# Kernel optimization log

Hardware: AMD Instinct MI355X
Metric: run time of the kernel (lower is better)

The kernel has to match this reference:

```python
import jax, jax.numpy as jnp
import numpy as np

N = 8192   # nodes per graph batch
D = 128    # node_feat_dim
E = 131072 # edges per graph batch
B = 64     # graphs per batch


def _linear_init(k, fin, fout):
    s = 1.0 / np.sqrt(fin)
    kw, kb = jax.random.split(k)
    W = jax.random.uniform(kw, (fin, fout), jnp.float32, -s, s)
    b = jax.random.uniform(kb, (fout,), jnp.float32, -s, s)
    return W, b


def setup_inputs() -> dict:
    key = jax.random.key(0)
    ks = jax.random.split(key, 10)
    x1 = jax.random.normal(ks[0], (N, D), jnp.float32)
    x2 = jax.random.normal(ks[1], (N, D), jnp.float32)
    edge_index1 = jax.random.randint(ks[2], (2, E), 0, N)
    edge_index2 = jax.random.randint(ks[3], (2, E), 0, N)
    # block-contiguous graph ids; every graph id present on both sides
    batch = jnp.arange(N, dtype=jnp.int32) // (N // B)
    mW1, mb1 = _linear_init(ks[4], 2 * D, 512)
    mW2, mb2 = _linear_init(ks[5], 512, 256)  # 256 == 2*D (update_net constraint)
    uW1, ub1 = _linear_init(ks[6], 4 * D, 512)
    uW2, ub2 = _linear_init(ks[7], 512, 256)
    uW3, ub3 = _linear_init(ks[8], 256, D)
    return dict(x1=x1, edge_index1=edge_index1, batch1=batch,
                x2=x2, edge_index2=edge_index2, batch2=batch,
                mW1=mW1, mb1=mb1, mW2=mW2, mb2=mb2,
                uW1=uW1, ub1=ub1, uW2=uW2, ub2=ub2, uW3=uW3, ub3=ub3)


def _message_aggr(x, edge_index, mW1, mb1, mW2, mb2):
    tgt, src = edge_index[0], edge_index[1]
    inp = jnp.concatenate([x[src], x[tgt]], axis=-1)          # [E, 2D]
    msg = jax.nn.relu(inp @ mW1 + mb1) @ mW2 + mb2            # [E, 2D]
    return jax.ops.segment_sum(msg, tgt, num_segments=x.shape[0])


def _cross_attention(x1, batch1, x2, batch2):
    scores = x1 @ x2.T                                        # [N1, N2]
    mask = batch1[:, None] == batch2[None, :]
    scores = jnp.where(mask, scores, -jnp.inf)
    att1 = x1 - jax.nn.softmax(scores, axis=1) @ x2
    att2 = x2 - jax.nn.softmax(scores, axis=0).T @ x1
    return att1, att2


def _node_update(x, messages, attentions, uW1, ub1, uW2, ub2, uW3, ub3):
    u = jnp.concatenate([messages, attentions, x], axis=-1)   # [N, 4D]
    h = jax.nn.relu(u @ uW1 + ub1)
    h = jax.nn.relu(h @ uW2 + ub2)
    return x + h @ uW3 + ub3                                  # residual update


def reference(x1, edge_index1, batch1, x2, edge_index2, batch2,
              mW1, mb1, mW2, mb2, uW1, ub1, uW2, ub2, uW3, ub3):
    m1 = _message_aggr(x1, edge_index1, mW1, mb1, mW2, mb2)
    m2 = _message_aggr(x2, edge_index2, mW1, mb1, mW2, mb2)
    a1, a2 = _cross_attention(x1, batch1, x2, batch2)
    new_x1 = _node_update(x1, m1, a1, uW1, ub1, uW2, ub2, uW3, ub3)
    new_x2 = _node_update(x2, m2, a2, uW1, ub1, uW2, ub2, uW3, ub3)
    return new_x1, new_x2
```

## Files before the change

kernel.cpp:

```cpp
#include <hip/hip_runtime.h>
#include <stdint.h>


typedef unsigned short u16;
typedef __bf16 bf16x8 __attribute__((ext_vector_type(8)));
typedef float f32x4 __attribute__((ext_vector_type(4)));

#define NN 8192
#define DD 128
#define EE 131072
#define GS 128
#define NG 64

__device__ __forceinline__ float bf2f(u16 u){
  return __uint_as_float(((uint32_t)u) << 16);
}
__device__ __forceinline__ u16 f2bf(float f){
  uint32_t x = __float_as_uint(f);
  return (u16)((x + 0x7fffu + ((x >> 16) & 1u)) >> 16);
}
__device__ __forceinline__ void gload16(const u16* g, u16* l){
  __builtin_amdgcn_global_load_lds(
      (const __attribute__((address_space(1))) uint32_t*)(uintptr_t)g,
      (__attribute__((address_space(3))) uint32_t*)(uintptr_t)l, 16, 0, 0);
}
template<int N>
__device__ __forceinline__ void wbar(){
  if constexpr (N == 0)      asm volatile("s_waitcnt vmcnt(0)" ::: "memory");
  else if constexpr (N == 1) asm volatile("s_waitcnt vmcnt(1)" ::: "memory");
  else if constexpr (N == 2) asm volatile("s_waitcnt vmcnt(2)" ::: "memory");
  else if constexpr (N == 4) asm volatile("s_waitcnt vmcnt(4)" ::: "memory");
  __builtin_amdgcn_s_barrier();
  __builtin_amdgcn_sched_barrier(0);
}
__device__ __forceinline__ void bar(){
  __builtin_amdgcn_s_barrier();
  __builtin_amdgcn_sched_barrier(0);
}

template<bool DEGBIAS, typename OT>
__device__ __forceinline__ void gemm_body(
    const u16* __restrict__ A, int lda,
    const u16* __restrict__ Wt, const float* __restrict__ bias,
    const int* __restrict__ deg,
    OT* __restrict__ out, int ldc, int K, int bx, int by,
    u16* __restrict__ sh, int t)
{
  u16* As0 = sh;         u16* Bs0 = sh + 4096;
  u16* As1 = sh + 8192;  u16* Bs1 = sh + 12288;
  const int brow = by << 7, bcol = bx << 7;
  const int w = t >> 6, lane = t & 63;
  const int rb = (w >> 1) << 6, cb = (w & 1) << 6;
  const int lr = lane & 15, lq = lane >> 4;

  f32x4 acc[4][4];
  #pragma unroll
  for (int i = 0; i < 4; i++)
    #pragma unroll
    for (int j = 0; j < 4; j++) acc[i][j] = (f32x4){0.f, 0.f, 0.f, 0.f};

  const int s0 = t, s1 = t + 256;
  const int sw0 = (((s0 & 3) ^ ((s0 >> 2) & 3)) << 3);
  const int sw1 = (((s1 & 3) ^ ((s1 >> 2) & 3)) << 3);
  const u16* Ag0 = A  + (size_t)(brow + (s0 >> 2)) * lda + sw0;
  const u16* Ag1 = A  + (size_t)(brow + (s1 >> 2)) * lda + sw1;
  const u16* Bg0 = Wt + (size_t)(bcol + (s0 >> 2)) * K   + sw0;
  const u16* Bg1 = Wt + (size_t)(bcol + (s1 >> 2)) * K   + sw1;
  const int d0 = s0 << 3, d1 = s1 << 3;

  auto stage = [&](int kb, u16* Al, u16* Bl){
    gload16(Ag0 + kb, Al + d0);
    gload16(Ag1 + kb, Al + d1);
    gload16(Bg0 + kb, Bl + d0);
    gload16(Bg1 + kb, Bl + d1);
  };
  const int swr = ((lq ^ (lr & 3)) << 3);
  auto compute = [&](const u16* Asb, const u16* Bsb){
    bf16x8 af[4], bfr[4];
    #pragma unroll
    for (int mi = 0; mi < 4; mi++)
      af[mi] = *(const bf16x8*)&Asb[(rb + mi * 16 + lr) * 32 + swr];
    #pragma unroll
    for (int ni = 0; ni < 4; ni++)
      bfr[ni] = *(const bf16x8*)&Bsb[(cb + ni * 16 + lr) * 32 + swr];
    #pragma unroll
    for (int mi = 0; mi < 4; mi++)
      #pragma unroll
      for (int ni = 0; ni < 4; ni++)
        acc[mi][ni] = __builtin_amdgcn_mfma_f32_16x16x32_bf16(af[mi], bfr[ni], acc[mi][ni], 0, 0, 0);
  };

  stage(0, As0, Bs0);
  const int half = K >> 6;
  for (int i2 = 0; i2 < half; i2++){
    const int kb = i2 << 6;
    stage(kb + 32, As1, Bs1);
    wbar<4>();
    compute(As0, Bs0);
    bar();
    if (i2 + 1 < half){
      stage(kb + 64, As0, Bs0);
      wbar<4>();
    } else {
      wbar<0>();
    }
    compute(As1, Bs1);
    bar();
  }

  #pragma unroll
  for (int mi = 0; mi < 4; mi++)
    #pragma unroll
    for (int ni = 0; ni < 4; ni++)
      #pragma unroll
      for (int rr = 0; rr < 4; rr++){
        int grow = brow + rb + mi * 16 + lq * 4 + rr;
        int gcol = bcol + cb + ni * 16 + lr;
        float v = acc[mi][ni][rr];
        if (bias) v += DEGBIAS ? (float)deg[grow] * bias[gcol] : bias[gcol];
        out[(size_t)grow * ldc + gcol] = (OT)f2bf(v);
      }
}

__device__ __forceinline__ void pq_gemm(
    const u16* __restrict__ A, const u16* __restrict__ Wt,
    const float* __restrict__ bias, u16* __restrict__ out,
    int bx, int by, u16* __restrict__ sh, int t)
{
  u16* As = sh;
  u16* Bs = sh + 16384;
  const int brow = by << 7, bcol = bx << 7;
  const int w = t >> 6, lane = t & 63;
  const int rb = (w >> 1) << 6, cb = (w & 1) << 6;
  const int lr = lane & 15, lq = lane >> 4;

  #pragma unroll
  for (int i = 0; i < 8; i++){
    int sg = i * 256 + t;
    int r = sg >> 4, p = sg & 15;
    int l = p ^ (r & 7);
    gload16(A  + (size_t)(brow + r) * 128 + (l << 3), As + sg * 8);
    gload16(Wt + (size_t)(bcol + r) * 128 + (l << 3), Bs + sg * 8);
  }
  wbar<0>();

  f32x4 acc[4][4];
  #pragma unroll
  for (int i = 0; i < 4; i++)
    #pragma unroll
    for (int j = 0; j < 4; j++) acc[i][j] = (f32x4){0.f, 0.f, 0.f, 0.f};

  #pragma unroll
  for (int kb = 0; kb < 4; kb++){
    bf16x8 af[4], bfr[4];
    #pragma unroll
    for (int mi = 0; mi < 4; mi++){
      int row = rb + mi * 16 + lr;
      af[mi] = *(const bf16x8*)&As[(row << 7) + ((((kb << 2) | lq) ^ (row & 7)) << 3)];
    }
    #pragma unroll
    for (int ni = 0; ni < 4; ni++){
      int row = cb + ni * 16 + lr;
      bfr[ni] = *(const bf16x8*)&Bs[(row << 7) + ((((kb << 2) | lq) ^ (row & 7)) << 3)];
    }
    #pragma unroll
    for (int mi = 0; mi < 4; mi++)
      #pragma unroll
      for (int ni = 0; ni < 4; ni++)
        acc[mi][ni] = __builtin_amdgcn_mfma_f32_16x16x32_bf16(af[mi], bfr[ni], acc[mi][ni], 0, 0, 0);
  }

  #pragma unroll
  for (int mi = 0; mi < 4; mi++)
    #pragma unroll
    for (int ni = 0; ni < 4; ni++)
      #pragma unroll
      for (int rr = 0; rr < 4; rr++){
        int grow = brow + rb + mi * 16 + lq * 4 + rr;
        int gcol = bcol + cb + ni * 16 + lr;
        out[(size_t)grow * 1024 + gcol] = f2bf(acc[mi][ni][rr] + bias[gcol]);
      }
}

__global__ __launch_bounds__(256)
void pre_k(const float* __restrict__ mW1, const float* __restrict__ mb1,
           const float* __restrict__ mW2, const float* __restrict__ uW1,
           const float* __restrict__ uW2, const float* __restrict__ uW3,
           const float* __restrict__ x1, const float* __restrict__ x2,
           const int* __restrict__ ei1, const int* __restrict__ ei2,
           u16* __restrict__ WtPQ, float* __restrict__ bPQ,
           u16* __restrict__ Wtm2, u16* __restrict__ Wtu1,
           u16* __restrict__ Wtu2, u16* __restrict__ Wtu3,
           u16* __restrict__ xb, u16* __restrict__ xt,
           u16* __restrict__ U, int* __restrict__ deg)
{
  __shared__ u16 T[8704];
  int b = blockIdx.x, t = threadIdx.x;
  if (b < 168){
    const float* srcs[6] = {mW1, mW1 + 128 * 512, mW2, uW1, uW2, uW3};
    u16* dsts[6] = {WtPQ, WtPQ + 512 * 128, Wtm2, Wtu1, Wtu2, Wtu3};
    const int ldSs[6] = {512, 512, 256, 512, 256, 128};
    const int ldDs[6] = {128, 128, 512, 512, 512, 256};
    const int jb[7]   = {0, 16, 32, 64, 128, 160, 168};
    int j = 0;
    while (b >= jb[j + 1]) j++;
    const int l = b - jb[j];
    const int ldS = ldSs[j], ldD = ldDs[j];
    const int ntc = ldS >> 6;
    const int k0 = (l / ntc) << 6, c0 = (l % ntc) << 6;
    const float* S = srcs[j];
    u16* D = dsts[j];
    #pragma unroll
    for (int i = 0; i < 4; i++){
      int s = i * 256 + t;
      int r = s >> 4, c4 = (s & 15) << 2;
      float4 v = *(const float4*)&S[(size_t)(k0 + r) * ldS + c0 + c4];
      uint2 pk;
      pk.x = (uint32_t)f2bf(v.x) | ((uint32_t)f2bf(v.y) << 16);
      pk.y = (uint32_t)f2bf(v.z) | ((uint32_t)f2bf(v.w) << 16);
      *(uint2*)&T[r * 68 + c4] = pk;
    }
    __syncthreads();
    #pragma unroll
    for (int i = 0; i < 4; i++){
      int s = i * 256 + t;
      int c = s >> 4, k4 = (s & 15) << 2;
      uint32_t a0 = T[(k4 + 0) * 68 + c];
      uint32_t a1 = T[(k4 + 1) * 68 + c];
      uint32_t a2 = T[(k4 + 2) * 68 + c];
      uint32_t a3 = T[(k4 + 3) * 68 + c];
      uint2 pk; pk.x = a0 | (a1 << 16); pk.y = a2 | (a3 << 16);
      *(uint2*)&D[(size_t)(c0 + c) * ldD + k0 + k4] = pk;
    }
  } else if (b == 168){
    #pragma unroll
    for (int i = 0; i < 4; i++){
      int idx = i * 256 + t;
      bPQ[idx] = (idx < 512) ? 0.f : mb1[idx - 512];
    }
  } else if (b < 2217){
    int a = b - 169;
    int side = a >> 10, blk = a & 1023;
    const float* x = side ? x2 : x1;
    int i4 = blk * 256 + t;
    float4 v = *(const float4*)&x[(size_t)i4 * 4];
    uint2 pk;
    pk.x = (uint32_t)f2bf(v.x) | ((uint32_t)f2bf(v.y) << 16);
    pk.y = (uint32_t)f2bf(v.z) | ((uint32_t)f2bf(v.w) << 16);
    *(uint2*)&xb[(size_t)side * NN * DD + (size_t)i4 * 4] = pk;
    int n = i4 >> 5, d = (i4 << 2) & 127;
    *(uint2*)&U[((size_t)side * NN + n) * 512 + 384 + d] = pk;
  } else if (b < 2473){
    int a = b - 2217;
    int side = a >> 7, blk = a & 127;
    const float* x = side ? x2 : x1;
    u16* dst = xt + (size_t)side * DD * NN;
    const int n0 = blk * 64;
    #pragma unroll
    for (int i = 0; i < 8; i++){
      int s = i * 256 + t;
      int r = s >> 5, c4 = (s & 31) << 2;
      float4 v = *(const float4*)&x[(size_t)(n0 + r) * DD + c4];
      uint2 pk;
      pk.x = (uint32_t)f2bf(v.x) | ((uint32_t)f2bf(v.y) << 16);
      pk.y = (uint32_t)f2bf(v.z) | ((uint32_t)f2bf(v.w) << 16);
      *(uint2*)&T[r * 136 + c4] = pk;
    }
    __syncthreads();
    #pragma unroll
    for (int i = 0; i < 8; i++){
      int s = i * 256 + t;
      int d = s >> 4, n4 = (s & 15) << 2;
      uint32_t a0 = T[(n4 + 0) * 136 + d];
      uint32_t a1 = T[(n4 + 1) * 136 + d];
      uint32_t a2 = T[(n4 + 2) * 136 + d];
      uint32_t a3 = T[(n4 + 3) * 136 + d];
      uint2 pk; pk.x = a0 | (a1 << 16); pk.y = a2 | (a3 << 16);
      *(uint2*)(dst + (size_t)d * NN + n0 + n4) = pk;
    }
  } else {
    int a = b - 2473;
    int side = a >> 9, blk = a & 511;
    const int* ei = side ? ei2 : ei1;
    int e = blk * 256 + t;
    atomicAdd(&deg[side * NN + ei[e]], 1);
  }
}

__global__ __launch_bounds__(256)
void scan_k(const int* __restrict__ deg,
            int* __restrict__ offs1, int* __restrict__ cur1,
            int* __restrict__ offs2, int* __restrict__ cur2){
  const int* d = deg + blockIdx.x * NN;
  int* offs = blockIdx.x ? offs2 : offs1;
  int* cur  = blockIdx.x ? cur2  : cur1;
  __shared__ int part[256];
  const int t = threadIdx.x;
  const int base = t * 32;
  int loc[32];
  int s = 0;
  #pragma unroll
  for (int i = 0; i < 32; i++){ loc[i] = s; s += d[base + i]; }
  part[t] = s;
  __syncthreads();
  for (int off = 1; off < 256; off <<= 1){
    int v = (t >= off) ? part[t - off] : 0;
    __syncthreads();
    part[t] += v;
    __syncthreads();
  }
  int pre = (t == 0) ? 0 : part[t - 1];
  #pragma unroll
  for (int i = 0; i < 32; i++){
    int o = pre + loc[i];
    offs[base + i] = o;
    cur[base + i]  = o;
  }
  if (t == 255) offs[NN] = part[255];
}

__global__ __launch_bounds__(256)
void mid_k(const u16* __restrict__ xb, const u16* __restrict__ WtPQ,
           const float* __restrict__ bPQ, u16* __restrict__ PQ,
           const int* __restrict__ ei1, const int* __restrict__ ei2,
           int* __restrict__ cur1, int* __restrict__ cur2,
           int* __restrict__ srt1, int* __restrict__ srt2)
{
  __shared__ u16 sh[32768];
  const int b = blockIdx.x, t = threadIdx.x;
  if (b < 1024){
    pq_gemm(xb, WtPQ, bPQ, PQ, b >> 7, b & 127, sh, t);
  } else {
    int a = b - 1024;
    int side = a >> 9, blk = a & 511;
    const int* ei = side ? ei2 : ei1;
    int* cur = side ? cur2 : cur1;
    int* srt = side ? srt2 : srt1;
    int e = blk * 256 + t;
    int tgt = ei[e], src = ei[EE + e];
    int p = atomicAdd(&cur[tgt], 1);
    srt[p] = src;
  }
}

__global__ __launch_bounds__(256)
void gather_k(const int* __restrict__ offs1, const int* __restrict__ srt1,
              const int* __restrict__ offs2, const int* __restrict__ srt2,
              const u16* __restrict__ PQ, u16* __restrict__ S)
{
  const int side = blockIdx.y;
  const int* offs = side ? offs2 : offs1;
  const int* srt  = side ? srt2  : srt1;
  const u16* base = PQ + (size_t)side * NN * 1024;
  u16* Sb = S + (size_t)side * NN * 512;

  const int node = (blockIdx.x << 2) + (threadIdx.x >> 6);
  const int lane = threadIdx.x & 63;
  const int beg = offs[node], end = offs[node + 1];
  const u16* lbase = base + (lane << 3);

  uint4 qv = *(const uint4*)(base + (size_t)node * 1024 + 512 + (lane << 3));
  float q[8];
  {
    uint32_t qw[4] = {qv.x, qv.y, qv.z, qv.w};
    #pragma unroll
    for (int i = 0; i < 4; i++){
      q[i * 2]     = bf2f((u16)(qw[i] & 0xffffu));
      q[i * 2 + 1] = bf2f((u16)(qw[i] >> 16));
    }
  }
  float acc[8] = {0.f,0.f,0.f,0.f,0.f,0.f,0.f,0.f};

  int e = beg;
  for (; e + 15 < end; e += 16){
    int sx[16];
    #pragma unroll
    for (int i = 0; i < 16; i++) sx[i] = srt[e + i];
    uint4 pv[16];
    #pragma unroll
    for (int i = 0; i < 16; i++)
      pv[i] = *(const uint4*)(lbase + (size_t)sx[i] * 1024);
    #pragma unroll
    for (int i = 0; i < 16; i++){
      uint32_t w0[4] = {pv[i].x, pv[i].y, pv[i].z, pv[i].w};
      #pragma unroll
      for (int j = 0; j < 4; j++){
        acc[j*2]   += fmaxf(bf2f((u16)(w0[j] & 0xffffu)) + q[j*2],   0.f);
        acc[j*2+1] += fmaxf(bf2f((u16)(w0[j] >> 16))     + q[j*2+1], 0.f);
      }
    }
  }
  for (; e + 7 < end; e += 8){
    int sx[8];
    #pragma unroll
    for (int i = 0; i < 8; i++) sx[i] = srt[e + i];
    uint4 pv[8];
    #pragma unroll
    for (int i = 0; i < 8; i++)
      pv[i] = *(const uint4*)(lbase + (size_t)sx[i] * 1024);
    #pragma unroll
    for (int i = 0; i < 8; i++){
      uint32_t w0[4] = {pv[i].x, pv[i].y, pv[i].z, pv[i].w};
      #pragma unroll
      for (int j = 0; j < 4; j++){
        acc[j*2]   += fmaxf(bf2f((u16)(w0[j] & 0xffffu)) + q[j*2],   0.f);
        acc[j*2+1] += fmaxf(bf2f((u16)(w0[j] >> 16))     + q[j*2+1], 0.f);
      }
    }
  }
  for (; e + 3 < end; e += 4){
    int sx[4];
    #pragma unroll
    for (int i = 0; i < 4; i++) sx[i] = srt[e + i];
    uint4 pv[4];
    #pragma unroll
    for (int i = 0; i < 4; i++)
      pv[i] = *(const uint4*)(lbase + (size_t)sx[i] * 1024);
    #pragma unroll
    for (int i = 0; i < 4; i++){
      uint32_t w0[4] = {pv[i].x, pv[i].y, pv[i].z, pv[i].w};
      #pragma unroll
      for (int j = 0; j < 4; j++){
        acc[j*2]   += fmaxf(bf2f((u16)(w0[j] & 0xffffu)) + q[j*2],   0.f);
        acc[j*2+1] += fmaxf(bf2f((u16)(w0[j] >> 16))     + q[j*2+1], 0.f);
      }
    }
  }
  for (; e < end; e++){
    int sA = srt[e];
    uint4 pA = *(const uint4*)(lbase + (size_t)sA * 1024);
    uint32_t aw[4] = {pA.x, pA.y, pA.z, pA.w};
    #pragma unroll
    for (int i = 0; i < 4; i++){
      acc[i*2]   += fmaxf(bf2f((u16)(aw[i] & 0xffffu)) + q[i*2],   0.f);
      acc[i*2+1] += fmaxf(bf2f((u16)(aw[i] >> 16))     + q[i*2+1], 0.f);
    }
  }
  uint4 pk;
  pk.x = (uint32_t)f2bf(acc[0]) | ((uint32_t)f2bf(acc[1]) << 16);
  pk.y = (uint32_t)f2bf(acc[2]) | ((uint32_t)f2bf(acc[3]) << 16);
  pk.z = (uint32_t)f2bf(acc[4]) | ((uint32_t)f2bf(acc[5]) << 16);
  pk.w = (uint32_t)f2bf(acc[6]) | ((uint32_t)f2bf(acc[7]) << 16);
  *(uint4*)(Sb + (size_t)node * 512 + (lane << 3)) = pk;
}

__global__ __launch_bounds__(256)
void msgattn_k(const u16* __restrict__ S, const u16* __restrict__ Wtm2,
               const float* __restrict__ mb2, const int* __restrict__ deg,
               const u16* __restrict__ xb, const u16* __restrict__ xt,
               u16* __restrict__ U)
{
  __shared__ u16 sh[26112];
  const int b = blockIdx.x, t = threadIdx.x;
  if (b < 256){
    gemm_body<true,u16>(S, 512, Wtm2, mb2, deg,
                        U, 512, 512, b >> 7, b & 127, sh, t);
    return;
  }
  const int a = b - 256;
  const int side = a >> 7;
  const int g = a & 63, h = (a >> 6) & 1;
  const u16* Xa = xb + (size_t)side * NN * DD;
  const u16* Xb = xb + (size_t)(1 - side) * NN * DD;
  const u16* Xt = xt + (size_t)(1 - side) * DD * NN;
  u16* Uside = U + (size_t)side * NN * 512;

  u16* XaS = sh;
  u16* XbS = sh + 8704;

  const int w = t >> 6, lane = t & 63;
  const int lr = lane & 15, lq = lane >> 4;

  {
    const u16* sa = Xa + ((size_t)g * GS + h * 64) * DD;
    #pragma unroll
    for (int i = 0; i < 4; i++){
      int s = i * 256 + t; int r = s >> 4, c8 = (s & 15) << 3;
      *(uint4*)&XaS[r * 136 + c8] = *(const uint4*)(sa + (size_t)r * DD + c8);
    }
    const u16* sb = Xb + (size_t)g * GS * DD;
    #pragma unroll
    for (int i = 0; i < 8; i++){
      int s = i * 256 + t; int r = s >> 4, c8 = (s & 15) << 3;
      *(uint4*)&XbS[r * 136 + c8] = *(const uint4*)(sb + (size_t)r * DD + c8);
    }
  }
  __syncthreads();

  f32x4 sc[8];
  #pragma unroll
  for (int ct = 0; ct < 8; ct++) sc[ct] = (f32x4){0.f, 0.f, 0.f, 0.f};
  #pragma unroll
  for (int kb = 0; kb < 4; kb++){
    bf16x8 aa = *(const bf16x8*)&XaS[(w * 16 + lr) * 136 + kb * 32 + (lq << 3)];
    #pragma unroll
    for (int ct = 0; ct < 8; ct++){
      bf16x8 bb = *(const bf16x8*)&XbS[(ct * 16 + lr) * 136 + kb * 32 + (lq << 3)];
      sc[ct] = __builtin_amdgcn_mfma_f32_16x16x32_bf16(aa, bb, sc[ct], 0, 0, 0);
    }
  }
  float inv[4];
  #pragma unroll
  for (int rr = 0; rr < 4; rr++){
    float m = sc[0][rr];
    #pragma unroll
    for (int ct = 1; ct < 8; ct++) m = fmaxf(m, sc[ct][rr]);
    #pragma unroll
    for (int sh_ = 1; sh_ < 16; sh_ <<= 1) m = fmaxf(m, __shfl_xor(m, sh_, 64));
    float s = 0.f;
    #pragma unroll
    for (int ct = 0; ct < 8; ct++){
      float e = __expf(sc[ct][rr] - m);
      sc[ct][rr] = e; s += e;
    }
    #pragma unroll
    for (int sh_ = 1; sh_ < 16; sh_ <<= 1) s += __shfl_xor(s, sh_, 64);
    inv[rr] = 1.f / s;
  }
  #pragma unroll
  for (int ct = 0; ct < 8; ct++)
    #pragma unroll
    for (int rr = 0; rr < 4; rr++)
      XaS[(w * 16 + lq * 4 + rr) * 136 + ct * 16 + lr] = f2bf(sc[ct][rr] * inv[rr]);
  __syncthreads();

  f32x4 o[8];
  #pragma unroll
  for (int ct = 0; ct < 8; ct++) o[ct] = (f32x4){0.f, 0.f, 0.f, 0.f};
  #pragma unroll
  for (int kb = 0; kb < 4; kb++){
    bf16x8 aa = *(const bf16x8*)&XaS[(w * 16 + lr) * 136 + kb * 32 + (lq << 3)];
    #pragma unroll
    for (int ct = 0; ct < 8; ct++){
      bf16x8 bb = *(const bf16x8*)(Xt + (size_t)(ct * 16 + lr) * NN + g * GS + kb * 32 + (lq << 3));
      o[ct] = __builtin_amdgcn_mfma_f32_16x16x32_bf16(aa, bb, o[ct], 0, 0, 0);
    }
  }
  const u16* XaG = Xa + ((size_t)g * GS + h * 64) * DD;
  #pragma unroll
  for (int ct = 0; ct < 8; ct++)
    #pragma unroll
    for (int rr = 0; rr < 4; rr++){
      int row = w * 16 + lq * 4 + rr, col = ct * 16 + lr;
      float xa = bf2f(XaG[(size_t)row * DD + col]);
      Uside[((size_t)g * GS + h * 64 + row) * 512 + 256 + col] = f2bf(xa - o[ct][rr]);
    }
}

__global__ __launch_bounds__(512)
void upd_k(const u16* __restrict__ U,
           const u16* __restrict__ Wtu1, const float* __restrict__ ub1,
           const u16* __restrict__ Wtu2, const float* __restrict__ ub2,
           const u16* __restrict__ Wtu3, const float* __restrict__ ub3,
           const float* __restrict__ x1, const float* __restrict__ x2,
           float* __restrict__ out)
{
  __shared__ u16 sh[66560];
  u16* H1s  = sh;
  u16* H2s  = sh + 33280;
  u16* Bst0 = sh + 50176;
  u16* Bst1 = sh + 58368;

  const int t = threadIdx.x;
  const int w = t >> 6, lane = t & 63;
  const int wr = w >> 2, wc = w & 3;
  const int lr = lane & 15, lq = lane >> 4;
  const int r0 = blockIdx.x << 6;

  const int sB0 = t, sB1 = t + 512;
  const int cB0 = sB0 >> 2, cB1 = sB1 >> 2;
  const int swB0 = (((sB0 & 3) ^ (cB0 & 3)) << 3);
  const int swB1 = (((sB1 & 3) ^ (cB1 & 3)) << 3);
  const int swr = ((lq ^ (lr & 3)) << 3);

  f32x4 acc[2][4];
  auto zacc = [&](){
    #pragma unroll
    for (int i = 0; i < 2; i++)
      #pragma unroll
      for (int j = 0; j < 4; j++) acc[i][j] = (f32x4){0.f, 0.f, 0.f, 0.f};
  };

  bf16x8 afA[2], afB[2];
  auto ldA = [&](int kb, bf16x8 (&af)[2]){
    #pragma unroll
    for (int mi = 0; mi < 2; mi++)
      af[mi] = *(const bf16x8*)&U[(size_t)(r0 + wr * 32 + mi * 16 + lr) * 512 + kb + (lq << 3)];
  };
  auto compA = [&](const bf16x8 (&af)[2], const u16* Bsb){
    bf16x8 bfv[4];
    #pragma unroll
    for (int ct = 0; ct < 4; ct++)
      bfv[ct] = *(const bf16x8*)&Bsb[(wc * 64 + ct * 16 + lr) * 32 + swr];
    #pragma unroll
    for (int mi = 0; mi < 2; mi++)
      #pragma unroll
      for (int ct = 0; ct < 4; ct++)
        acc[mi][ct] = __builtin_amdgcn_mfma_f32_16x16x32_bf16(af[mi], bfv[ct], acc[mi][ct], 0, 0, 0);
  };
  for (int hN = 0; hN < 2; hN++){
    zacc();
    auto stB = [&](int kb, u16* dst){
      gload16(Wtu1 + (size_t)(hN * 256 + cB0) * 512 + kb + swB0, dst + sB0 * 8);
      gload16(Wtu1 + (size_t)(hN * 256 + cB1) * 512 + kb + swB1, dst + sB1 * 8);
    };
    stB(0, Bst0);
    ldA(0, afA);
    for (int i2 = 0; i2 < 8; i2++){
      const int kb = i2 << 6;
      stB(kb + 32, Bst1); ldA(kb + 32, afB);
      wbar<4>();
      compA(afA, Bst0);
      bar();
      if (i2 < 7){
        stB(kb + 64, Bst0); ldA(kb + 64, afA);
        wbar<4>();
      } else {
        wbar<0>();
      }
      compA(afB, Bst1);
      bar();
    }
    #pragma unroll
    for (int mi = 0; mi < 2; mi++)
      #pragma unroll
      for (int ct = 0; ct < 4; ct++)
        #pragma unroll
        for (int rr = 0; rr < 4; rr++){
          int row = wr * 32 + mi * 16 + lq * 4 + rr;
          int col = wc * 64 + ct * 16 + lr;
          float v = acc[mi][ct][rr] + ub1[hN * 256 + col];
          H1s[row * 520 + hN * 256 + col] = f2bf(fmaxf(v, 0.f));
        }
  }
  __syncthreads();

  zacc();
  {
    auto stB = [&](int kb, u16* dst){
      gload16(Wtu2 + (size_t)cB0 * 512 + kb + swB0, dst + sB0 * 8);
      gload16(Wtu2 + (size_t)cB1 * 512 + kb + swB1, dst + sB1 * 8);
    };
    auto comp = [&](int kb, const u16* Bsb){
      bf16x8 af[2], bfv[4];
      #pragma unroll
      for (int mi = 0; mi < 2; mi++)
        af[mi] = *(const bf16x8*)&H1s[(wr * 32 + mi * 16 + lr) * 520 + kb + (lq << 3)];
      #pragma unroll
      for (int ct = 0; ct < 4; ct++)
        bfv[ct] = *(const bf16x8*)&Bsb[(wc * 64 + ct * 16 + lr) * 32 + swr];
      #pragma unroll
      for (int mi = 0; mi < 2; mi++)
        #pragma unroll
        for (int ct = 0; ct < 4; ct++)
          acc[mi][ct] = __builtin_amdgcn_mfma_f32_16x16x32_bf16(af[mi], bfv[ct], acc[mi][ct], 0, 0, 0);
    };
    stB(0, Bst0);
    for (int i2 = 0; i2 < 8; i2++){
      const int kb = i2 << 6;
      stB(kb + 32, Bst1);
      wbar<2>();
      comp(kb, Bst0);
      bar();
      if (i2 < 7){
        stB(kb + 64, Bst0);
        wbar<2>();
      } else {
        wbar<0>();
      }
      comp(kb + 32, Bst1);
      bar();
    }
    #pragma unroll
    for (int mi = 0; mi < 2; mi++)
      #pragma unroll
      for (int ct = 0; ct < 4; ct++)
        #pragma unroll
        for (int rr = 0; rr < 4; rr++){
          int row = wr * 32 + mi * 16 + lq * 4 + rr;
          int col = wc * 64 + ct * 16 + lr;
          H2s[row * 264 + col] = f2bf(fmaxf(acc[mi][ct][rr] + ub2[col], 0.f));
        }
  }
  __syncthreads();

  zacc();
  {
    auto stB = [&](int kb, u16* dst){
      gload16(Wtu3 + (size_t)cB0 * 256 + kb + swB0, dst + sB0 * 8);
    };
    auto comp = [&](int kb, const u16* Bsb){
      bf16x8 af[2], bfv[2];
      #pragma unroll
      for (int mi = 0; mi < 2; mi++)
        af[mi] = *(const bf16x8*)&H2s[(wr * 32 + mi * 16 + lr) * 264 + kb + (lq << 3)];
      #pragma unroll
      for (int ct = 0; ct < 2; ct++)
        bfv[ct] = *(const bf16x8*)&Bsb[(wc * 32 + ct * 16 + lr) * 32 + swr];
      #pragma unroll
      for (int mi = 0; mi < 2; mi++)
        #pragma unroll
        for (int ct = 0; ct < 2; ct++)
          acc[mi][ct] = __builtin_amdgcn_mfma_f32_16x16x32_bf16(af[mi], bfv[ct], acc[mi][ct], 0, 0, 0);
    };
    stB(0, Bst0);
    for (int i2 = 0; i2 < 4; i2++){
      const int kb = i2 << 6;
      stB(kb + 32, Bst1);
      wbar<1>();
      comp(kb, Bst0);
      bar();
      if (i2 < 3){
        stB(kb + 64, Bst0);
        wbar<1>();
      } else {
        wbar<0>();
      }
      comp(kb + 32, Bst1);
      bar();
    }
    #pragma unroll
    for (int mi = 0; mi < 2; mi++)
      #pragma unroll
      for (int ct = 0; ct < 2; ct++)
        #pragma unroll
        for (int rr = 0; rr < 4; rr++){
          int row = wr * 32 + mi * 16 + lq * 4 + rr;
          int col = wc * 32 + ct * 16 + lr;
          int grow = r0 + row;
          const float* rp = (grow < NN) ? x1 : x2;
          float v = acc[mi][ct][rr] + ub3[col]
                  + rp[(size_t)(grow & (NN - 1)) * 128 + col];
          out[(size_t)grow * 128 + col] = v;
        }
  }
}

extern "C" void kernel_launch(void* const* d_in, const int* in_sizes, int n_in,
                              void* d_out, int out_size, void* d_ws, size_t ws_size,
                              hipStream_t stream)
{
  const float* x1  = (const float*)d_in[0];
  const int*   ei1 = (const int*)  d_in[1];
  const float* x2  = (const float*)d_in[3];
  const int*   ei2 = (const int*)  d_in[4];
  const float* mW1 = (const float*)d_in[6];
  const float* mb1 = (const float*)d_in[7];
  const float* mW2 = (const float*)d_in[8];
  const float* mb2 = (const float*)d_in[9];
  const float* uW1 = (const float*)d_in[10];
  const float* ub1 = (const float*)d_in[11];
  const float* uW2 = (const float*)d_in[12];
  const float* ub2 = (const float*)d_in[13];
  const float* uW3 = (const float*)d_in[14];
  const float* ub3 = (const float*)d_in[15];
  float* out = (float*)d_out;

  char* w = (char*)d_ws;
  auto alloc = [&](size_t b){ char* p = w; w += (b + 255) & ~(size_t)255; return p; };
  u16*  S    = (u16*)alloc((size_t)2 * NN * 512 * 2);
  u16*  PQ   = (u16*)alloc((size_t)2 * NN * 1024 * 2);
  u16*  xb   = (u16*)alloc((size_t)2 * NN * DD * 2);
  u16*  xt   = (u16*)alloc((size_t)2 * DD * NN * 2);
  u16*  U    = (u16*)alloc((size_t)2 * NN * 512 * 2);
  int*  deg  = (int*)alloc((size_t)2 * NN * 4);
  int*  offs1 = (int*)alloc((NN + 1) * 4);
  int*  offs2 = (int*)alloc((NN + 1) * 4);
  int*  cur1  = (int*)alloc(NN * 4);
  int*  cur2  = (int*)alloc(NN * 4);
  int*  srt1  = (int*)alloc((size_t)EE * 4);
  int*  srt2  = (int*)alloc((size_t)EE * 4);
  u16*  WtPQ = (u16*)alloc(1024 * 128 * 2);
  float* bPQ = (float*)alloc(1024 * 4);
  u16*  Wtm2 = (u16*)alloc(256 * 512 * 2);
  u16*  Wtu1 = (u16*)alloc(512 * 512 * 2);
  u16*  Wtu2 = (u16*)alloc(256 * 512 * 2);
  u16*  Wtu3 = (u16*)alloc(128 * 256 * 2);

  hipMemsetAsync(deg, 0, (size_t)2 * NN * 4, stream);

  pre_k<<<3497, 256, 0, stream>>>(
      mW1, mb1, mW2, uW1, uW2, uW3, x1, x2, ei1, ei2,
      WtPQ, bPQ, Wtm2, Wtu1, Wtu2, Wtu3, xb, xt, U, deg);

  scan_k<<<2, 256, 0, stream>>>(deg, offs1, cur1, offs2, cur2);

  mid_k<<<2048, 256, 0, stream>>>(xb, WtPQ, bPQ, PQ, ei1, ei2,
                                  cur1, cur2, srt1, srt2);

  gather_k<<<dim3(NN / 4, 2), 256, 0, stream>>>(offs1, srt1, offs2, srt2, PQ, S);

  msgattn_k<<<512, 256, 0, stream>>>(S, Wtm2, mb2, deg, xb, xt, U);

  upd_k<<<256, 512, 0, stream>>>(U, Wtu1, ub1, Wtu2, ub2, Wtu3, ub3,
                                 x1, x2, out);
}
```

Measured before the change: 220.2 us.

## Fuse message GEMM into update kernel and move attention into mid kernel

Removes the msgattn kernel. The cross-attention blocks are appended to the mid_k launch so they run alongside the PQ GEMM and the edge sort. The message second-layer GEMM (S x Wtm2 plus degree-scaled bias) now runs at the start of upd_k, which writes U rows and then reuses them for the update MLP. This saves a launch and lets attention overlap the gather, at the cost of more work inside upd_k. Each upd_k block writes U through global memory and then reads it back within the same block, relying on that visibility being correct.

```diff
diff --git a/kernel.cpp b/kernel.cpp
--- a/kernel.cpp
+++ b/kernel.cpp
@@ -36,90 +36,6 @@
 __device__ __forceinline__ void bar(){
   __builtin_amdgcn_s_barrier();
   __builtin_amdgcn_sched_barrier(0);
-}
-
-template<bool DEGBIAS, typename OT>
-__device__ __forceinline__ void gemm_body(
-    const u16* __restrict__ A, int lda,
-    const u16* __restrict__ Wt, const float* __restrict__ bias,
-    const int* __restrict__ deg,
-    OT* __restrict__ out, int ldc, int K, int bx, int by,
-    u16* __restrict__ sh, int t)
-{
-  u16* As0 = sh;         u16* Bs0 = sh + 4096;
-  u16* As1 = sh + 8192;  u16* Bs1 = sh + 12288;
-  const int brow = by << 7, bcol = bx << 7;
-  const int w = t >> 6, lane = t & 63;
-  const int rb = (w >> 1) << 6, cb = (w & 1) << 6;
-  const int lr = lane & 15, lq = lane >> 4;
-
-  f32x4 acc[4][4];
-  #pragma unroll
-  for (int i = 0; i < 4; i++)
-    #pragma unroll
-    for (int j = 0; j < 4; j++) acc[i][j] = (f32x4){0.f, 0.f, 0.f, 0.f};
-
-  const int s0 = t, s1 = t + 256;
-  const int sw0 = (((s0 & 3) ^ ((s0 >> 2) & 3)) << 3);
-  const int sw1 = (((s1 & 3) ^ ((s1 >> 2) & 3)) << 3);
-  const u16* Ag0 = A  + (size_t)(brow + (s0 >> 2)) * lda + sw0;
-  const u16* Ag1 = A  + (size_t)(brow + (s1 >> 2)) * lda + sw1;
-  const u16* Bg0 = Wt + (size_t)(bcol + (s0 >> 2)) * K   + sw0;
-  const u16* Bg1 = Wt + (size_t)(bcol + (s1 >> 2)) * K   + sw1;
-  const int d0 = s0 << 3, d1 = s1 << 3;
-
-  auto stage = [&](int kb, u16* Al, u16* Bl){
-    gload16(Ag0 + kb, Al + d0);
-    gload16(Ag1 + kb, Al + d1);
-    gload16(Bg0 + kb, Bl + d0);
-    gload16(Bg1 + kb, Bl + d1);
-  };
-  const int swr = ((lq ^ (lr & 3)) << 3);
-  auto compute = [&](const u16* Asb, const u16* Bsb){
-    bf16x8 af[4], bfr[4];
-    #pragma unroll
-    for (int mi = 0; mi < 4; mi++)
-      af[mi] = *(const bf16x8*)&Asb[(rb + mi * 16 + lr) * 32 + swr];
-    #pragma unroll
-    for (int ni = 0; ni < 4; ni++)
-      bfr[ni] = *(const bf16x8*)&Bsb[(cb + ni * 16 + lr) * 32 + swr];
-    #pragma unroll
-    for (int mi = 0; mi < 4; mi++)
-      #pragma unroll
-      for (int ni = 0; ni < 4; ni++)
-        acc[mi][ni] = __builtin_amdgcn_mfma_f32_16x16x32_bf16(af[mi], bfr[ni], acc[mi][ni], 0, 0, 0);
-  };
-
-  stage(0, As0, Bs0);
-  const int half = K >> 6;
-  for (int i2 = 0; i2 < half; i2++){
-    const int kb = i2 << 6;
-    stage(kb + 32, As1, Bs1);
-    wbar<4>();
-    compute(As0, Bs0);
-    bar();
-    if (i2 + 1 < half){
-      stage(kb + 64, As0, Bs0);
-      wbar<4>();
-    } else {
-      wbar<0>();
-    }
-    compute(As1, Bs1);
-    bar();
-  }
-
-  #pragma unroll
-  for (int mi = 0; mi < 4; mi++)
-    #pragma unroll
-    for (int ni = 0; ni < 4; ni++)
-      #pragma unroll
-      for (int rr = 0; rr < 4; rr++){
-        int grow = brow + rb + mi * 16 + lq * 4 + rr;
-        int gcol = bcol + cb + ni * 16 + lr;
-        float v = acc[mi][ni][rr];
-        if (bias) v += DEGBIAS ? (float)deg[grow] * bias[gcol] : bias[gcol];
-        out[(size_t)grow * ldc + gcol] = (OT)f2bf(v);
-      }
 }
 
 __device__ __forceinline__ void pq_gemm(
@@ -324,13 +240,16 @@
            const float* __restrict__ bPQ, u16* __restrict__ PQ,
            const int* __restrict__ ei1, const int* __restrict__ ei2,
            int* __restrict__ cur1, int* __restrict__ cur2,
-           int* __restrict__ srt1, int* __restrict__ srt2)
+           int* __restrict__ srt1, int* __restrict__ srt2,
+           const u16* __restrict__ xt, u16* __restrict__ U)
 {
   __shared__ u16 sh[32768];
   const int b = blockIdx.x, t = threadIdx.x;
   if (b < 1024){
     pq_gemm(xb, WtPQ, bPQ, PQ, b >> 7, b & 127, sh, t);
-  } else {
+    return;
+  }
+  if (b < 2048){
     int a = b - 1024;
     int side = a >> 9, blk = a & 511;
     const int* ei = side ? ei2 : ei1;
@@ -340,7 +259,96 @@
     int tgt = ei[e], src = ei[EE + e];
     int p = atomicAdd(&cur[tgt], 1);
     srt[p] = src;
-  }
+    return;
+  }
+  const int a = b - 2048;
+  const int side = a >> 7;
+  const int g = a & 63, h = (a >> 6) & 1;
+  const u16* Xa = xb + (size_t)side * NN * DD;
+  const u16* Xb = xb + (size_t)(1 - side) * NN * DD;
+  const u16* Xt = xt + (size_t)(1 - side) * DD * NN;
+  u16* Uside = U + (size_t)side * NN * 512;
+
+  u16* XaS = sh;
+  u16* XbS = sh + 8704;
+
+  const int w = t >> 6, lane = t & 63;
+  const int lr = lane & 15, lq = lane >> 4;
+
+  {
+    const u16* sa = Xa + ((size_t)g * GS + h * 64) * DD;
+    #pragma unroll
+    for (int i = 0; i < 4; i++){
+      int s = i * 256 + t; int r = s >> 4, c8 = (s & 15) << 3;
+      *(uint4*)&XaS[r * 136 + c8] = *(const uint4*)(sa + (size_t)r * DD + c8);
+    }
+    const u16* sb = Xb + (size_t)g * GS * DD;
+    #pragma unroll
+    for (int i = 0; i < 8; i++){
+      int s = i * 256 + t; int r = s >> 4, c8 = (s & 15) << 3;
+      *(uint4*)&XbS[r * 136 + c8] = *(const uint4*)(sb + (size_t)r * DD + c8);
+    }
+  }
+  __syncthreads();
+
+  f32x4 sc[8];
+  #pragma unroll
+  for (int ct = 0; ct < 8; ct++) sc[ct] = (f32x4){0.f, 0.f, 0.f, 0.f};
+  #pragma unroll
+  for (int kb = 0; kb < 4; kb++){
+    bf16x8 aa = *(const bf16x8*)&XaS[(w * 16 + lr) * 136 + kb * 32 + (lq << 3)];
+    #pragma unroll
+    for (int ct = 0; ct < 8; ct++){
+      bf16x8 bb = *(const bf16x8*)&XbS[(ct * 16 + lr) * 136 + kb * 32 + (lq << 3)];
+      sc[ct] = __builtin_amdgcn_mfma_f32_16x16x32_bf16(aa, bb, sc[ct], 0, 0, 0);
+    }
+  }
+  float inv[4];
+  #pragma unroll
+  for (int rr = 0; rr < 4; rr++){
+    float m = sc[0][rr];
+    #pragma unroll
+    for (int ct = 1; ct < 8; ct++) m = fmaxf(m, sc[ct][rr]);
+    #pragma unroll
+    for (int sh_ = 1; sh_ < 16; sh_ <<= 1) m = fmaxf(m, __shfl_xor(m, sh_, 64));
+    float s = 0.f;
+    #pragma unroll
+    for (int ct = 0; ct < 8; ct++){
+      float e = __expf(sc[ct][rr] - m);
+      sc[ct][rr] = e; s += e;
+    }
+    #pragma unroll
+    for (int sh_ = 1; sh_ < 16; sh_ <<= 1) s += __shfl_xor(s, sh_, 64);
+    inv[rr] = 1.f / s;
+  }
+  #pragma unroll
+  for (int ct = 0; ct < 8; ct++)
+    #pragma unroll
+    for (int rr = 0; rr < 4; rr++)
+      XaS[(w * 16 + lq * 4 + rr) * 136 + ct * 16 + lr] = f2bf(sc[ct][rr] * inv[rr]);
+  __syncthreads();
+
+  f32x4 o[8];
+  #pragma unroll
+  for (int ct = 0; ct < 8; ct++) o[ct] = (f32x4){0.f, 0.f, 0.f, 0.f};
+  #pragma unroll
+  for (int kb = 0; kb < 4; kb++){
+    bf16x8 aa = *(const bf16x8*)&XaS[(w * 16 + lr) * 136 + kb * 32 + (lq << 3)];
+    #pragma unroll
+    for (int ct = 0; ct < 8; ct++){
+      bf16x8 bb = *(const bf16x8*)(Xt + (size_t)(ct * 16 + lr) * NN + g * GS + kb * 32 + (lq << 3));
+      o[ct] = __builtin_amdgcn_mfma_f32_16x16x32_bf16(aa, bb, o[ct], 0, 0, 0);
+    }
+  }
+  const u16* XaG = Xa + ((size_t)g * GS + h * 64) * DD;
+  #pragma unroll
+  for (int ct = 0; ct < 8; ct++)
+    #pragma unroll
+    for (int rr = 0; rr < 4; rr++){
+      int row = w * 16 + lq * 4 + rr, col = ct * 16 + lr;
+      float xa = bf2f(XaG[(size_t)row * DD + col]);
+      Uside[((size_t)g * GS + h * 64 + row) * 512 + 256 + col] = f2bf(xa - o[ct][rr]);
+    }
 }
 
 __global__ __launch_bounds__(256)
@@ -444,111 +452,10 @@
   *(uint4*)(Sb + (size_t)node * 512 + (lane << 3)) = pk;
 }
 
-__global__ __launch_bounds__(256)
-void msgattn_k(const u16* __restrict__ S, const u16* __restrict__ Wtm2,
-               const float* __restrict__ mb2, const int* __restrict__ deg,
-               const u16* __restrict__ xb, const u16* __restrict__ xt,
-               u16* __restrict__ U)
-{
-  __shared__ u16 sh[26112];
-  const int b = blockIdx.x, t = threadIdx.x;
-  if (b < 256){
-    gemm_body<true,u16>(S, 512, Wtm2, mb2, deg,
-                        U, 512, 512, b >> 7, b & 127, sh, t);
-    return;
-  }
-  const int a = b - 256;
-  const int side = a >> 7;
-  const int g = a & 63, h = (a >> 6) & 1;
-  const u16* Xa = xb + (size_t)side * NN * DD;
-  const u16* Xb = xb + (size_t)(1 - side) * NN * DD;
-  const u16* Xt = xt + (size_t)(1 - side) * DD * NN;
-  u16* Uside = U + (size_t)side * NN * 512;
-
-  u16* XaS = sh;
-  u16* XbS = sh + 8704;
-
-  const int w = t >> 6, lane = t & 63;
-  const int lr = lane & 15, lq = lane >> 4;
-
-  {
-    const u16* sa = Xa + ((size_t)g * GS + h * 64) * DD;
-    #pragma unroll
-    for (int i = 0; i < 4; i++){
-      int s = i * 256 + t; int r = s >> 4, c8 = (s & 15) << 3;
-      *(uint4*)&XaS[r * 136 + c8] = *(const uint4*)(sa + (size_t)r * DD + c8);
-    }
-    const u16* sb = Xb + (size_t)g * GS * DD;
-    #pragma unroll
-    for (int i = 0; i < 8; i++){
-      int s = i * 256 + t; int r = s >> 4, c8 = (s & 15) << 3;
-      *(uint4*)&XbS[r * 136 + c8] = *(const uint4*)(sb + (size_t)r * DD + c8);
-    }
-  }
-  __syncthreads();
-
-  f32x4 sc[8];
-  #pragma unroll
-  for (int ct = 0; ct < 8; ct++) sc[ct] = (f32x4){0.f, 0.f, 0.f, 0.f};
-  #pragma unroll
-  for (int kb = 0; kb < 4; kb++){
-    bf16x8 aa = *(const bf16x8*)&XaS[(w * 16 + lr) * 136 + kb * 32 + (lq << 3)];
-    #pragma unroll
-    for (int ct = 0; ct < 8; ct++){
-      bf16x8 bb = *(const bf16x8*)&XbS[(ct * 16 + lr) * 136 + kb * 32 + (lq << 3)];
-      sc[ct] = __builtin_amdgcn_mfma_f32_16x16x32_bf16(aa, bb, sc[ct], 0, 0, 0);
-    }
-  }
-  float inv[4];
-  #pragma unroll
-  for (int rr = 0; rr < 4; rr++){
-    float m = sc[0][rr];
-    #pragma unroll
-    for (int ct = 1; ct < 8; ct++) m = fmaxf(m, sc[ct][rr]);
-    #pragma unroll
-    for (int sh_ = 1; sh_ < 16; sh_ <<= 1) m = fmaxf(m, __shfl_xor(m, sh_, 64));
-    float s = 0.f;
-    #pragma unroll
-    for (int ct = 0; ct < 8; ct++){
-      float e = __expf(sc[ct][rr] - m);
-      sc[ct][rr] = e; s += e;
-    }
-    #pragma unroll
-    for (int sh_ = 1; sh_ < 16; sh_ <<= 1) s += __shfl_xor(s, sh_, 64);
-    inv[rr] = 1.f / s;
-  }
-  #pragma unroll
-  for (int ct = 0; ct < 8; ct++)
-    #pragma unroll
-    for (int rr = 0; rr < 4; rr++)
-      XaS[(w * 16 + lq * 4 + rr) * 136 + ct * 16 + lr] = f2bf(sc[ct][rr] * inv[rr]);
-  __syncthreads();
-
-  f32x4 o[8];
-  #pragma unroll
-  for (int ct = 0; ct < 8; ct++) o[ct] = (f32x4){0.f, 0.f, 0.f, 0.f};
-  #pragma unroll
-  for (int kb = 0; kb < 4; kb++){
-    bf16x8 aa = *(const bf16x8*)&XaS[(w * 16 + lr) * 136 + kb * 32 + (lq << 3)];
-    #pragma unroll
-    for (int ct = 0; ct < 8; ct++){
-      bf16x8 bb = *(const bf16x8*)(Xt + (size_t)(ct * 16 + lr) * NN + g * GS + kb * 32 + (lq << 3));
-      o[ct] = __builtin_amdgcn_mfma_f32_16x16x32_bf16(aa, bb, o[ct], 0, 0, 0);
-    }
-  }
-  const u16* XaG = Xa + ((size_t)g * GS + h * 64) * DD;
-  #pragma unroll
-  for (int ct = 0; ct < 8; ct++)
-    #pragma unroll
-    for (int rr = 0; rr < 4; rr++){
-      int row = w * 16 + lq * 4 + rr, col = ct * 16 + lr;
-      float xa = bf2f(XaG[(size_t)row * DD + col]);
-      Uside[((size_t)g * GS + h * 64 + row) * 512 + 256 + col] = f2bf(xa - o[ct][rr]);
-    }
-}
-
 __global__ __launch_bounds__(512)
-void upd_k(const u16* __restrict__ U,
+void upd_k(const u16* __restrict__ Sg,
+           const u16* __restrict__ Wtm2, const float* __restrict__ mb2,
+           const int* __restrict__ deg, u16* __restrict__ U,
            const u16* __restrict__ Wtu1, const float* __restrict__ ub1,
            const u16* __restrict__ Wtu2, const float* __restrict__ ub2,
            const u16* __restrict__ Wtu3, const float* __restrict__ ub3,
@@ -580,23 +487,66 @@
       #pragma unroll
       for (int j = 0; j < 4; j++) acc[i][j] = (f32x4){0.f, 0.f, 0.f, 0.f};
   };
-
   bf16x8 afA[2], afB[2];
+  auto compA = [&](const bf16x8 (&af)[2], const u16* Bsb){
+    bf16x8 bfv[4];
+    #pragma unroll
+    for (int ct = 0; ct < 4; ct++)
+      bfv[ct] = *(const bf16x8*)&Bsb[(wc * 64 + ct * 16 + lr) * 32 + swr];
+    #pragma unroll
+    for (int mi = 0; mi < 2; mi++)
+      #pragma unroll
+      for (int ct = 0; ct < 4; ct++)
+        acc[mi][ct] = __builtin_amdgcn_mfma_f32_16x16x32_bf16(af[mi], bfv[ct], acc[mi][ct], 0, 0, 0);
+  };
+
+  zacc();
+  {
+    auto ldS = [&](int kb, bf16x8 (&af)[2]){
+      #pragma unroll
+      for (int mi = 0; mi < 2; mi++)
+        af[mi] = *(const bf16x8*)&Sg[(size_t)(r0 + wr * 32 + mi * 16 + lr) * 512 + kb + (lq << 3)];
+    };
+    auto stB = [&](int kb, u16* dst){
+      gload16(Wtm2 + (size_t)cB0 * 512 + kb + swB0, dst + sB0 * 8);
+      gload16(Wtm2 + (size_t)cB1 * 512 + kb + swB1, dst + sB1 * 8);
+    };
+    stB(0, Bst0);
+    ldS(0, afA);
+    for (int i2 = 0; i2 < 8; i2++){
+      const int kb = i2 << 6;
+      stB(kb + 32, Bst1); ldS(kb + 32, afB);
+      wbar<4>();
+      compA(afA, Bst0);
+      bar();
+      if (i2 < 7){
+        stB(kb + 64, Bst0); ldS(kb + 64, afA);
+        wbar<4>();
+      } else {
+        wbar<0>();
+      }
+      compA(afB, Bst1);
+      bar();
+    }
+    #pragma unroll
+    for (int mi = 0; mi < 2; mi++)
+      #pragma unroll
+      for (int ct = 0; ct < 4; ct++)
+        #pragma unroll
+        for (int rr = 0; rr < 4; rr++){
+          int row = wr * 32 + mi * 16 + lq * 4 + rr;
+          int col = wc * 64 + ct * 16 + lr;
+          int grow = r0 + row;
+          float v = acc[mi][ct][rr] + (float)deg[grow] * mb2[col];
+          U[(size_t)grow * 512 + col] = f2bf(v);
+        }
+  }
+  wbar<0>();
+
   auto ldA = [&](int kb, bf16x8 (&af)[2]){
     #pragma unroll
     for (int mi = 0; mi < 2; mi++)
       af[mi] = *(const bf16x8*)&U[(size_t)(r0 + wr * 32 + mi * 16 + lr) * 512 + kb + (lq << 3)];
-  };
-  auto compA = [&](const bf16x8 (&af)[2], const u16* Bsb){
-    bf16x8 bfv[4];
-    #pragma unroll
-    for (int ct = 0; ct < 4; ct++)
-      bfv[ct] = *(const bf16x8*)&Bsb[(wc * 64 + ct * 16 + lr) * 32 + swr];
-    #pragma unroll
-    for (int mi = 0; mi < 2; mi++)
-      #pragma unroll
-      for (int ct = 0; ct < 4; ct++)
-        acc[mi][ct] = __builtin_amdgcn_mfma_f32_16x16x32_bf16(af[mi], bfv[ct], acc[mi][ct], 0, 0, 0);
   };
   for (int hN = 0; hN < 2; hN++){
     zacc();
@@ -785,13 +735,12 @@
 
   scan_k<<<2, 256, 0, stream>>>(deg, offs1, cur1, offs2, cur2);
 
-  mid_k<<<2048, 256, 0, stream>>>(xb, WtPQ, bPQ, PQ, ei1, ei2,
-                                  cur1, cur2, srt1, srt2);
+  mid_k<<<2304, 256, 0, stream>>>(xb, WtPQ, bPQ, PQ, ei1, ei2,
+                                  cur1, cur2, srt1, srt2, xt, U);
 
   gather_k<<<dim3(NN / 4, 2), 256, 0, stream>>>(offs1, srt1, offs2, srt2, PQ, S);
 
-  msgattn_k<<<512, 256, 0, stream>>>(S, Wtm2, mb2, deg, xb, xt, U);
-
-  upd_k<<<256, 512, 0, stream>>>(U, Wtu1, ub1, Wtu2, ub2, Wtu3, ub3,
+  upd_k<<<256, 512, 0, stream>>>(S, Wtm2, mb2, deg, U,
+                                 Wtu1, ub1, Wtu2, ub2, Wtu3, ub3,
                                  x1, x2, out);
 }
```

New measurement: 220.0 us (median of 3 runs). No clear change (-0.1%).
